# Performance work log

Hardware: AMD Instinct MI355X
Metric: run time of the kernel (lower is better)

Reference implementation:

```python
import jax, jax.numpy as jnp
import numpy as np

HEADS = 8
DIM_HEAD = 64
MAX_POS = 512


def setup_inputs() -> dict:
    key = jax.random.key(0)
    ks = jax.random.split(key, 10)
    b, n, dim, inner = 4, 1024, 512, HEADS * DIM_HEAD
    w = lambda k, shape: jax.random.normal(k, shape, jnp.float32) * 0.02
    return {
        "x": jax.random.normal(ks[0], (b, n, dim, 2), jnp.float32),
        "wq_r": w(ks[1], (dim, inner)),
        "wq_i": w(ks[2], (dim, inner)),
        "wkv_r": w(ks[3], (dim, 2 * inner)),
        "wkv_i": w(ks[4], (dim, 2 * inner)),
        "wo_r": w(ks[5], (inner, dim)),
        "wo_i": w(ks[6], (inner, dim)),
        "bo_r": w(ks[7], (dim,)),
        "bo_i": w(ks[8], (dim,)),
        "rel_emb": w(ks[9], (2 * MAX_POS + 1, DIM_HEAD)),
    }


def _clinear(t, Wr, Wi, br=None, bi=None):
    # complex linear: (a+ib)(Wr+iWi) = (aWr - bWi) + i(bWr + aWi)
    a, b = t[..., 0], t[..., 1]
    r = a @ Wr - b @ Wi
    i = b @ Wr + a @ Wi
    if br is not None:
        r = r + br
        i = i + bi
    return jnp.stack((r, i), axis=-1)


def _split_heads(t, h):
    # [b, n, h*d, 2] -> [b, h, n, d, 2]
    b, n, hd, c = t.shape
    return t.reshape(b, n, h, hd // h, c).transpose(0, 2, 1, 3, 4)


def reference(x, wq_r, wq_i, wkv_r, wkv_i, wo_r, wo_i, bo_r, bo_i, rel_emb):
    b, n = x.shape[0], x.shape[1]
    scale = DIM_HEAD ** (-0.5)

    q = _split_heads(_clinear(x, wq_r, wq_i), HEADS)          # [b,h,n,d,2]
    kv = _clinear(x, wkv_r, wkv_i)                            # [b,n,2*inner,2]
    k_, v_ = jnp.split(kv, 2, axis=-2)
    k = _split_heads(k_, HEADS)
    v = _split_heads(v_, HEADS)

    qr, qi = q[..., 0], q[..., 1]
    kr, ki = k[..., 0], k[..., 1]

    dots_r = (jnp.einsum('bhid,bhjd->bhij', qr, kr)
              - jnp.einsum('bhid,bhjd->bhij', qi, ki)) * scale
    dots_i = (jnp.einsum('bhid,bhjd->bhij', qr, ki)
              + jnp.einsum('bhid,bhjd->bhij', qi, kr)) * scale

    seq = jnp.arange(n)
    dist = jnp.clip(seq[:, None] - seq[None, :], -MAX_POS, MAX_POS) + MAX_POS  # [n,n]
    rel = rel_emb[dist]                                       # [n, n, d]
    dots_r = dots_r + jnp.einsum('bhnd,nrd->bhnr', qr, rel) * scale
    dots_i = dots_i + jnp.einsum('bhnd,nrd->bhnr', qi, rel) * scale

    # magnitude softmax over keys
    attn = jax.nn.softmax(jnp.sqrt(dots_r ** 2 + dots_i ** 2), axis=-1)  # [b,h,i,j]

    vr, vi = v[..., 0], v[..., 1]
    out_r = jnp.einsum('bhij,bhjd->bhid', attn, vr)
    out_i = jnp.einsum('bhij,bhjd->bhid', attn, vi)
    # [b,h,n,d] -> [b,n,h*d]
    out_r = out_r.transpose(0, 2, 1, 3).reshape(b, n, -1)
    out_i = out_i.transpose(0, 2, 1, 3).reshape(b, n, -1)
    out = jnp.stack((out_r, out_i), axis=-1)                  # [b,n,inner,2]

    # to_out (with bias); dropout prob 0 -> identity
    return _clinear(out, wo_r, wo_i, bo_r, bo_i)
```

## Files before the change

kernel.cpp:

```cpp
#include <hip/hip_runtime.h>
#include <hip/hip_bf16.h>


using bf16 = __bf16;
typedef __bf16 bf16x8 __attribute__((ext_vector_type(8)));
typedef float f32x4 __attribute__((ext_vector_type(4)));
typedef unsigned u32x4 __attribute__((ext_vector_type(4)));

#define MFMA16(a, b, c) __builtin_amdgcn_mfma_f32_16x16x32_bf16((a), (b), (c), 0, 0, 0)

__device__ __forceinline__ float ld_in(const void* p, long long i, int f32) {
  return f32 ? ((const float*)p)[i] : (float)((const bf16*)p)[i];
}

__device__ __forceinline__ void gl_lds16(const bf16* g, const bf16* l) {
  __builtin_amdgcn_global_load_lds(
      (const __attribute__((address_space(1))) void*)(unsigned long long)g,
      (__attribute__((address_space(3))) void*)(unsigned int)(unsigned long long)l,
      16, 0, 0);
}

template <int CTRL>
__device__ __forceinline__ float dpp_mv(float v) {
  int s = __builtin_bit_cast(int, v);
  return __builtin_bit_cast(float,
      __builtin_amdgcn_update_dpp(s, s, CTRL, 0xf, 0xf, false));
}
__device__ __forceinline__ float dpp_sum16(float v) {
  v += dpp_mv<0x121>(v);
  v += dpp_mv<0x122>(v);
  v += dpp_mv<0x124>(v);
  v += dpp_mv<0x128>(v);
  return v;
}

__device__ __forceinline__ unsigned pack_bf16(float lo, float hi) {
  unsigned a = (unsigned)__builtin_bit_cast(unsigned short, (bf16)lo);
  unsigned b = (unsigned)__builtin_bit_cast(unsigned short, (bf16)hi);
  return a | (b << 16);
}

__global__ __launch_bounds__(256) void k_diag(float* __restrict__ out, float v) {
  int idx = blockIdx.x * 256 + threadIdx.x;
  if (idx < 4194304) out[idx] = v;
}

__global__ void k_detect_all(
    const unsigned short* p0, const unsigned short* p1, const unsigned short* p2,
    const unsigned short* p3, const unsigned short* p4, const unsigned short* p5,
    const unsigned short* p6, const unsigned short* p7, const unsigned short* p8,
    const unsigned short* p9, int* __restrict__ flags) {
  static const int sizes[10] = {65536, 65536, 65536, 65536, 65536,
                                65536, 65536, 512, 512, 65536};
  const unsigned short* ptrs[10] = {p0, p1, p2, p3, p4, p5, p6, p7, p8, p9};
  __shared__ int cnt;
  if (threadIdx.x == 0) cnt = 0;
  __syncthreads();
  const int which = blockIdx.x;
  const unsigned short* p = ptrs[which];
  const int nhalf = sizes[which];
  const int ns = nhalf < 4096 ? nhalf : 4096;
  const int stp = nhalf / ns;
  int c = 0;
  for (int i = threadIdx.x; i < ns; i += 256) {
    const unsigned u = p[(size_t)i * stp];
    const unsigned e = (u >> 7) & 0xFF;
    if (e == 0xFF || (e < 64 && (u & 0x7FFF) != 0)) ++c;
  }
  atomicAdd(&cnt, c);
  __syncthreads();
  if (threadIdx.x == 0) flags[which] = (cnt > (ns >> 6)) ? 1 : 0;
}

__global__ __launch_bounds__(256) void k_build_all(
    const void* __restrict__ x,
    const void* __restrict__ wq_r, const void* __restrict__ wq_i,
    const void* __restrict__ wkv_r, const void* __restrict__ wkv_i,
    const void* __restrict__ wo_r, const void* __restrict__ wo_i,
    const void* __restrict__ rel,
    bf16* __restrict__ wct, bf16* __restrict__ wot,
    bf16* __restrict__ xd, bf16* __restrict__ rel_c,
    const int* __restrict__ flags) {
  __shared__ float tile[64][65];
  const int bid = blockIdx.x;
  const int t = threadIdx.x;
  if (bid < 1024) {
    const bool is_o = bid >= 768;
    const int lb = is_o ? bid - 768 : bid;
    const int k0 = (lb & 15) * 64;
    const int c0 = (lb >> 4) * 64;
    const int kk0 = k0 & 511;
    const bool hi = k0 >= 512;
    const void* src;
    int f, ld, scol;
    float sgn = 1.f;
    if (is_o) {
      ld = 512;
      if (c0 < 512) { scol = c0;       if (!hi) { src = wo_r; f = flags[5]; } else { src = wo_i; f = flags[6]; sgn = -1.f; } }
      else          { scol = c0 - 512; if (!hi) { src = wo_i; f = flags[6]; } else { src = wo_r; f = flags[5]; } }
    } else {
      ld = (c0 < 1024) ? 512 : 1024;
      if (c0 < 512)       { scol = c0;              if (!hi) { src = wq_r;  f = flags[1]; } else { src = wq_i;  f = flags[2]; sgn = -1.f; } }
      else if (c0 < 1024) { scol = c0 - 512;        if (!hi) { src = wq_i;  f = flags[2]; } else { src = wq_r;  f = flags[1]; } }
      else if (c0 < 1536) { scol = c0 - 1024;       if (!hi) { src = wkv_r; f = flags[3]; } else { src = wkv_i; f = flags[4]; sgn = -1.f; } }
      else if (c0 < 2048) { scol = c0 - 1536;       if (!hi) { src = wkv_i; f = flags[4]; } else { src = wkv_r; f = flags[3]; } }
      else if (c0 < 2560) { scol = c0 - 2048 + 512; if (!hi) { src = wkv_r; f = flags[3]; } else { src = wkv_i; f = flags[4]; sgn = -1.f; } }
      else                { scol = c0 - 2560 + 512; if (!hi) { src = wkv_i; f = flags[4]; } else { src = wkv_r; f = flags[3]; } }
    }
    const int cc = t & 63, rq = t >> 6;
#pragma unroll
    for (int rp = 0; rp < 16; ++rp) {
      const int rr = rp * 4 + rq;
      tile[rr][cc] = sgn * ld_in(src, (long long)(kk0 + rr) * ld + scol + cc, f);
    }
    __syncthreads();
    bf16* dst = is_o ? wot : wct;
    const int cr = t >> 3, kb = (t & 7) * 8;
#pragma unroll
    for (int p = 0; p < 2; ++p) {
      const int c = cr + p * 32;
      bf16x8 v;
#pragma unroll
      for (int e = 0; e < 8; ++e) v[e] = (bf16)tile[kb + e][c];
      *(bf16x8*)(dst + (size_t)(c0 + c) * 1024 + k0 + kb) = v;
    }
  } else if (bid < 9216) {
    const int f = flags[0];
    int idx = (bid - 1024) * 256 + t;
    int m = idx >> 9, j = idx & 511;
    long long base = (long long)m * 1024 + j * 2;
    xd[(size_t)m * 1024 + j] = (bf16)ld_in(x, base, f);
    xd[(size_t)m * 1024 + 512 + j] = (bf16)ld_in(x, base + 1, f);
  } else {
    const int f = flags[9];
    int idx = (bid - 9216) * 256 + t;
    if (idx < 65600) rel_c[idx] = (bf16)ld_in(rel, idx, f);
  }
}

template <int MODE, int BN>
__global__ __launch_bounds__(256) void k_gemm(
    const bf16* __restrict__ A, const bf16* __restrict__ Bt,
    bf16* __restrict__ C, float* __restrict__ Cf,
    bf16* __restrict__ Vtr, bf16* __restrict__ Vti,
    const int M, const int N, const int K,
    const void* __restrict__ bias_r, const void* __restrict__ bias_i,
    const int* __restrict__ flags) {
  constexpr int MT = (BN == 128) ? 4 : 2;
  __shared__ __align__(16) bf16 As[128 * 64];
  __shared__ __align__(16) bf16 Bs[BN * 64];
  const int tid = threadIdx.x;
  const int wave = tid >> 6, lane = tid & 63;
  const int lane15 = lane & 15, quad = lane >> 4;
  const int per = gridDim.x >> 3;
  const int s = (blockIdx.x & 7) * per + (blockIdx.x >> 3);
  const int nbx = N / BN;
  const int bm = (s / nbx) * 128, bn = (s % nbx) * BN;
  int wm, wn;
  if constexpr (BN == 128) { wm = (wave >> 1) * 64; wn = (wave & 1) * 64; }
  else                     { wm = wave * 32;        wn = 0; }
  const int sr = lane >> 3;
  const int scs = ((lane & 7) ^ sr) * 8;
  const int s7 = lane15 & 7;
  f32x4 acc[MT][4];
#pragma unroll
  for (int i = 0; i < MT; ++i)
#pragma unroll
    for (int j = 0; j < 4; ++j) acc[i][j] = (f32x4){0.f, 0.f, 0.f, 0.f};

  for (int k0 = 0; k0 < K; k0 += 64) {
#pragma unroll
    for (int p = 0; p < 4; ++p) {
      const int g = wave * 4 + p;
      gl_lds16(A + (size_t)(bm + g * 8 + sr) * K + k0 + scs, As + g * 512);
    }
    if constexpr (BN == 128) {
#pragma unroll
      for (int p = 0; p < 4; ++p) {
        const int g = wave * 4 + p;
        gl_lds16(Bt + (size_t)(bn + g * 8 + sr) * K + k0 + scs, Bs + g * 512);
      }
    } else {
#pragma unroll
      for (int p = 0; p < 2; ++p) {
        const int g = wave * 2 + p;
        gl_lds16(Bt + (size_t)(bn + g * 8 + sr) * K + k0 + scs, Bs + g * 512);
      }
    }
    __syncthreads();
#pragma unroll
    for (int kk = 0; kk < 2; ++kk) {
      const int go = ((kk * 4 + quad) ^ s7) * 8;
      bf16x8 af[MT], bfr[4];
#pragma unroll
      for (int mt = 0; mt < MT; ++mt)
        af[mt] = *(const bf16x8*)(As + (wm + mt * 16 + lane15) * 64 + go);
#pragma unroll
      for (int nt = 0; nt < 4; ++nt)
        bfr[nt] = *(const bf16x8*)(Bs + (wn + nt * 16 + lane15) * 64 + go);
#pragma unroll
      for (int mt = 0; mt < MT; ++mt)
#pragma unroll
        for (int nt = 0; nt < 4; ++nt) acc[mt][nt] = MFMA16(af[mt], bfr[nt], acc[mt][nt]);
    }
    __syncthreads();
  }

  if constexpr (MODE == 0) {
    if (bn < 2048) {
#pragma unroll
      for (int mt = 0; mt < MT; ++mt)
#pragma unroll
        for (int nt = 0; nt < 4; ++nt)
#pragma unroll
          for (int r = 0; r < 4; ++r) {
            const int m = bm + wm + mt * 16 + quad * 4 + r;
            const int n = bn + wn + nt * 16 + lane15;
            C[(size_t)m * 2048 + n] = (bf16)acc[mt][nt][r];
          }
    } else {
      const int hbase = bn - 2048 + wn;
      unsigned* vtp = (unsigned*)((hbase < 512) ? Vtr : Vti);
      const int dg0 = hbase & 511;
      const int bb = bm >> 10;
      const int jt = ((bm & 1023) >> 6) + (wm >> 6);
      const int bh = bb * 8 + (dg0 >> 6);
      unsigned* slab = vtp + (((size_t)(bh * 16 + jt)) << 11) + (quad * 16 + lane15) * 4;
#pragma unroll
      for (int nt = 0; nt < 4; ++nt)
#pragma unroll
        for (int hp = 0; hp < 2; ++hp) {
          u32x4 w;
#pragma unroll
          for (int r = 0; r < 4; ++r)
            w[r] = pack_bf16(acc[2 * hp][nt][r], acc[2 * hp + 1][nt][r]);
          *(u32x4*)(slab + nt * 512 + hp * 256) = w;
        }
    }
  } else {
    const int fbr = flags[7], fbi = flags[8];
#pragma unroll
    for (int mt = 0; mt < MT; ++mt)
#pragma unroll
      for (int nt = 0; nt < 4; ++nt)
#pragma unroll
        for (int r = 0; r < 4; ++r) {
          const int m = bm + wm + mt * 16 + quad * 4 + r;
          const int n = bn + wn + nt * 16 + lane15;
          float v = acc[mt][nt][r];
          const int c = (n < 512) ? n : n - 512;
          v += ld_in((n < 512) ? bias_r : bias_i, c, (n < 512) ? fbr : fbi);
          Cf[(size_t)m * 1024 + c * 2 + ((n < 512) ? 0 : 1)] = v;
        }
  }
}

__device__ __forceinline__ bf16x8 lds_frag72(const bf16* base, int row, int kofs) {
  return *(const bf16x8*)(base + row * 72 + kofs);
}

__global__ __launch_bounds__(256, 2) void k_attn(
    const bf16* __restrict__ C1, const bf16* __restrict__ vt_r, const bf16* __restrict__ vt_i,
    const bf16* __restrict__ rel, bf16* __restrict__ Oc) {
  __shared__ __align__(16) bf16 kr_s[64 * 72];
  __shared__ __align__(16) bf16 ki_s[64 * 72];
  __shared__ unsigned Gt32[4][1360];

  const int tid = threadIdx.x;
  const int wave = tid >> 6, lane = tid & 63;
  const int lane15 = lane & 15, quad = lane >> 4;
  const int qk0 = quad * 8;
  const int bid0 = blockIdx.x;
  const int bid = (bid0 & 7) * 64 + (bid0 >> 3);
  const int bh = bid >> 4, it = bid & 15;
  const int b = bh >> 3, h = bh & 7;
  const int i0 = it * 64;
  const int tq = tid >> 3;
  const int tc = (tid & 7) * 8;

  unsigned* const Gw = &Gt32[wave][0];

  const size_t qbase = (size_t)(b * 1024 + i0 + wave * 16 + lane15) * 2048 + h * 64;
  bf16x8 aqr[2], aqi[2], aqin[2];
  aqr[0] = *(const bf16x8*)(C1 + qbase + qk0);
  aqr[1] = *(const bf16x8*)(C1 + qbase + 32 + qk0);
  aqi[0] = *(const bf16x8*)(C1 + qbase + 512 + qk0);
  aqi[1] = *(const bf16x8*)(C1 + qbase + 512 + 32 + qk0);
#pragma unroll
  for (int c = 0; c < 2; ++c)
#pragma unroll
    for (int e = 0; e < 8; ++e) aqin[c][e] = (bf16)(-(float)aqi[c][e]);

  f32x4 o_r[4], o_i[4];
#pragma unroll
  for (int dt = 0; dt < 4; ++dt) { o_r[dt] = (f32x4){0.f,0.f,0.f,0.f}; o_i[dt] = (f32x4){0.f,0.f,0.f,0.f}; }
  f32x4 l_st = (f32x4){0.f, 0.f, 0.f, 0.f};

  bf16x8 pKr[2], pKi[2];
  auto issueK = [&](int jtn) {
    const int j0 = jtn * 64;
#pragma unroll
    for (int p = 0; p < 2; ++p) {
      const int row = p * 32 + tq;
      const size_t gbase = (size_t)(b * 1024 + j0 + row) * 2048 + h * 64 + tc;
      pKr[p] = *(const bf16x8*)(C1 + gbase + 1024);
      pKi[p] = *(const bf16x8*)(C1 + gbase + 1536);
    }
  };

  bf16x8 rb0[5], rb1[5];
  auto loadR = [&](int jtn) {
    const int t0w = 449 + i0 - jtn * 64 + wave * 16;
#pragma unroll
    for (int g = 0; g < 5; ++g) {
      int trw = t0w + g * 16 + lane15;
      trw = trw < 0 ? 0 : (trw > 1024 ? 1024 : trw);
      const bf16* rp = rel + (size_t)trw * 64;
      rb0[g] = *(const bf16x8*)(rp + qk0);
      rb1[g] = *(const bf16x8*)(rp + 32 + qk0);
    }
  };

  issueK(0);
  loadR(0);
  for (int jt = 0; jt < 16; ++jt) {
#pragma unroll
    for (int p = 0; p < 2; ++p) {
      const int row = p * 32 + tq;
      *(bf16x8*)(kr_s + row * 72 + tc) = pKr[p];
      *(bf16x8*)(ki_s + row * 72 + tc) = pKi[p];
    }
    __syncthreads();
    if (jt < 15) issueK(jt + 1);

#pragma unroll
    for (int g = 0; g < 5; ++g) {
      f32x4 gr = (f32x4){0.f,0.f,0.f,0.f}, gi = (f32x4){0.f,0.f,0.f,0.f};
      gr = MFMA16(aqr[0], rb0[g], gr);
      gr = MFMA16(aqr[1], rb1[g], gr);
      gi = MFMA16(aqi[0], rb0[g], gi);
      gi = MFMA16(aqi[1], rb1[g], gi);
      const int trow = (g * 16 + lane15) * 17;
#pragma unroll
      for (int r = 0; r < 4; ++r)
        Gw[trow + quad * 4 + r] = pack_bf16(gr[r], gi[r]);
    }

    if (jt < 15) loadR(jt + 1);

    f32x4 s_r[4], s_i[4];
#pragma unroll
    for (int ct = 0; ct < 4; ++ct) { s_r[ct] = (f32x4){0.f,0.f,0.f,0.f}; s_i[ct] = (f32x4){0.f,0.f,0.f,0.f}; }
    __builtin_amdgcn_s_setprio(1);
#pragma unroll
    for (int ct = 0; ct < 4; ++ct) {
      const int krow = ct * 16 + lane15;
      bf16x8 bkr0 = lds_frag72(kr_s, krow, qk0), bkr1 = lds_frag72(kr_s, krow, 32 + qk0);
      bf16x8 bki0 = lds_frag72(ki_s, krow, qk0), bki1 = lds_frag72(ki_s, krow, 32 + qk0);
      s_r[ct] = MFMA16(aqr[0], bkr0, s_r[ct]);
      s_r[ct] = MFMA16(aqr[1], bkr1, s_r[ct]);
      s_r[ct] = MFMA16(aqin[0], bki0, s_r[ct]);
      s_r[ct] = MFMA16(aqin[1], bki1, s_r[ct]);
      s_i[ct] = MFMA16(aqr[0], bki0, s_i[ct]);
      s_i[ct] = MFMA16(aqr[1], bki1, s_i[ct]);
      s_i[ct] = MFMA16(aqi[0], bkr0, s_i[ct]);
      s_i[ct] = MFMA16(aqi[1], bkr1, s_i[ct]);
    }
    __builtin_amdgcn_s_setprio(0);
    __syncthreads();

    const unsigned* vbr = (const unsigned*)vt_r + (((size_t)(bh * 16 + jt)) << 11) + lane * 4;
    const unsigned* vbi = (const unsigned*)vt_i + (((size_t)(bh * 16 + jt)) << 11) + lane * 4;
    bf16x8 vr0[4], vr1[4];
#pragma unroll
    for (int dt = 0; dt < 4; ++dt) {
      vr0[dt] = *(const bf16x8*)(vbr + dt * 512);
      vr1[dt] = *(const bf16x8*)(vbr + dt * 512 + 256);
    }

    float mag[4][4];
#pragma unroll
    for (int ct = 0; ct < 4; ++ct) {
      const int jj = ct * 16 + lane15;
#pragma unroll
      for (int r = 0; r < 4; ++r) {
        const int ii = quad * 4 + r;
        const unsigned gv = Gw[(ii - jj + 63) * 17 + ii];
        const float gr = __builtin_bit_cast(float, gv << 16);
        const float gi = __builtin_bit_cast(float, gv & 0xffff0000u);
        const float dr = s_r[ct][r] + gr;
        const float di = s_i[ct][r] + gi;
        mag[ct][r] = fminf(0.125f * sqrtf(dr * dr + di * di), 80.f);
      }
    }
#pragma unroll
    for (int r = 0; r < 4; ++r) {
      const int ii = quad * 4 + r;
      float pv[4];
#pragma unroll
      for (int ct = 0; ct < 4; ++ct) pv[ct] = __expf(mag[ct][r]);
      l_st[r] += (pv[0] + pv[1]) + (pv[2] + pv[3]);
      Gw[ii * 36 + lane15]      = pack_bf16(pv[0], pv[1]);
      Gw[ii * 36 + 16 + lane15] = pack_bf16(pv[2], pv[3]);
    }

    bf16x8 vi0[4], vi1[4];
#pragma unroll
    for (int dt = 0; dt < 4; ++dt) {
      vi0[dt] = *(const bf16x8*)(vbi + dt * 512);
      vi1[dt] = *(const bf16x8*)(vbi + dt * 512 + 256);
    }

    bf16x8 ap0 = *(const bf16x8*)((const bf16*)Gw + lane15 * 72 + quad * 8);
    bf16x8 ap1 = *(const bf16x8*)((const bf16*)Gw + lane15 * 72 + 32 + quad * 8);
    __builtin_amdgcn_s_setprio(1);
#pragma unroll
    for (int dt = 0; dt < 4; ++dt) {
      o_r[dt] = MFMA16(ap0, vr0[dt], o_r[dt]);
      o_r[dt] = MFMA16(ap1, vr1[dt], o_r[dt]);
    }
#pragma unroll
    for (int dt = 0; dt < 4; ++dt) {
      o_i[dt] = MFMA16(ap0, vi0[dt], o_i[dt]);
      o_i[dt] = MFMA16(ap1, vi1[dt], o_i[dt]);
    }
    __builtin_amdgcn_s_setprio(0);
  }

  const size_t obase = (size_t)(b * 1024 + i0 + wave * 16) * 1024 + h * 64;
#pragma unroll
  for (int r = 0; r < 4; ++r) {
    const float inv = 1.0f / dpp_sum16(l_st[r]);
    const int ii = quad * 4 + r;
#pragma unroll
    for (int dt = 0; dt < 4; ++dt) {
      Oc[obase + (size_t)ii * 1024 + dt * 16 + lane15] = (bf16)(o_r[dt][r] * inv);
      Oc[obase + (size_t)ii * 1024 + 512 + dt * 16 + lane15] = (bf16)(o_i[dt][r] * inv);
    }
  }
}

extern "C" void kernel_launch(void* const* d_in, const int* in_sizes, int n_in,
                              void* d_out, int out_size, void* d_ws, size_t ws_size,
                              hipStream_t stream) {
  float* out = (float*)d_out;

  if (n_in != 10) { k_diag<<<16384, 256, 0, stream>>>(out, 300000.f); return; }
  if (out_size != 4194304) { k_diag<<<16384, 256, 0, stream>>>(out, 400000.f); return; }
  static const int dict_sizes[10] = {4194304, 262144, 262144, 524288, 524288,
                                     262144, 262144, 512, 512, 65600};
  for (int i = 0; i < 10; ++i) {
    if (in_sizes[i] != dict_sizes[i]) { k_diag<<<16384, 256, 0, stream>>>(out, 200000.f); return; }
  }
  const size_t NEED = 50462888;
  if (ws_size < NEED) { k_diag<<<16384, 256, 0, stream>>>(out, 100000.f); return; }

  const void* x     = d_in[0];
  const void* wq_r  = d_in[1];
  const void* wq_i  = d_in[2];
  const void* wkv_r = d_in[3];
  const void* wkv_i = d_in[4];
  const void* wo_r  = d_in[5];
  const void* wo_i  = d_in[6];
  const void* bo_r  = d_in[7];
  const void* bo_i  = d_in[8];
  const void* rel   = d_in[9];

  char* ws = (char*)d_ws;
  bf16* C1   = (bf16*)(ws);
  bf16* Vtr  = (bf16*)(ws + 16777216);
  bf16* Vti  = (bf16*)(ws + 20971520);
  bf16* Xd   = (bf16*)(ws + 25165824);
  bf16* Oc   = (bf16*)(ws + 33554432);
  bf16* WcT  = (bf16*)(ws + 41943040);
  bf16* WoT  = (bf16*)(ws + 48234496);
  bf16* relc = (bf16*)(ws + 50331648);
  int*  flags= (int*)(ws + 50462848);

  k_detect_all<<<10, 256, 0, stream>>>(
      (const unsigned short*)x, (const unsigned short*)wq_r, (const unsigned short*)wq_i,
      (const unsigned short*)wkv_r, (const unsigned short*)wkv_i, (const unsigned short*)wo_r,
      (const unsigned short*)wo_i, (const unsigned short*)bo_r, (const unsigned short*)bo_i,
      (const unsigned short*)rel, flags);

  k_build_all<<<9473, 256, 0, stream>>>(x, wq_r, wq_i, wkv_r, wkv_i, wo_r, wo_i, rel,
                                        WcT, WoT, Xd, relc, flags);

  k_gemm<0, 128><<<768, 256, 0, stream>>>(Xd, WcT, C1, nullptr, Vtr, Vti,
                                          4096, 3072, 1024, nullptr, nullptr, flags);
  k_attn<<<512, 256, 0, stream>>>(C1, Vtr, Vti, relc, Oc);
  k_gemm<1, 64><<<512, 256, 0, stream>>>(Oc, WoT, nullptr, out, nullptr, nullptr,
                                         4096, 1024, 1024, bo_r, bo_i, flags);
}
```

Baseline: 223.4 us.

## Shrink output GEMM tiles, simplify softmax exponent, reduce dtype-probe sampling

New measurement: 221.7 us. No clear change (-0.8%).

```diff
diff --git a/kernel.cpp b/kernel.cpp
--- a/kernel.cpp
+++ b/kernel.cpp
@@ -59,7 +59,7 @@
   const int which = blockIdx.x;
   const unsigned short* p = ptrs[which];
   const int nhalf = sizes[which];
-  const int ns = nhalf < 4096 ? nhalf : 4096;
+  const int ns = nhalf < 1024 ? nhalf : 1024;
   const int stp = nhalf / ns;
   int c = 0;
   for (int i = threadIdx.x; i < ns; i += 256) {
@@ -138,7 +138,7 @@
   }
 }
 
-template <int MODE, int BN>
+template <int MODE, int BM, int BN>
 __global__ __launch_bounds__(256) void k_gemm(
     const bf16* __restrict__ A, const bf16* __restrict__ Bt,
     bf16* __restrict__ C, float* __restrict__ Cf,
@@ -146,8 +146,10 @@
     const int M, const int N, const int K,
     const void* __restrict__ bias_r, const void* __restrict__ bias_i,
     const int* __restrict__ flags) {
-  constexpr int MT = (BN == 128) ? 4 : 2;
-  __shared__ __align__(16) bf16 As[128 * 64];
+  constexpr int MT = (BM == 128 && BN == 128) ? 4 : (BM == 128 ? 2 : 1);
+  constexpr int APW = (BM / 8) / 4;
+  constexpr int BPW = (BN / 8) / 4;
+  __shared__ __align__(16) bf16 As[BM * 64];
   __shared__ __align__(16) bf16 Bs[BN * 64];
   const int tid = threadIdx.x;
   const int wave = tid >> 6, lane = tid & 63;
@@ -155,10 +157,11 @@
   const int per = gridDim.x >> 3;
   const int s = (blockIdx.x & 7) * per + (blockIdx.x >> 3);
   const int nbx = N / BN;
-  const int bm = (s / nbx) * 128, bn = (s % nbx) * BN;
+  const int bm = (s / nbx) * BM, bn = (s % nbx) * BN;
   int wm, wn;
-  if constexpr (BN == 128) { wm = (wave >> 1) * 64; wn = (wave & 1) * 64; }
-  else                     { wm = wave * 32;        wn = 0; }
+  if constexpr (BM == 128 && BN == 128) { wm = (wave >> 1) * 64; wn = (wave & 1) * 64; }
+  else if constexpr (BM == 128)         { wm = wave * 32;        wn = 0; }
+  else                                  { wm = wave * 16;        wn = 0; }
   const int sr = lane >> 3;
   const int scs = ((lane & 7) ^ sr) * 8;
   const int s7 = lane15 & 7;
@@ -170,22 +173,14 @@
 
   for (int k0 = 0; k0 < K; k0 += 64) {
 #pragma unroll
-    for (int p = 0; p < 4; ++p) {
-      const int g = wave * 4 + p;
+    for (int p = 0; p < APW; ++p) {
+      const int g = wave * APW + p;
       gl_lds16(A + (size_t)(bm + g * 8 + sr) * K + k0 + scs, As + g * 512);
     }
-    if constexpr (BN == 128) {
-#pragma unroll
-      for (int p = 0; p < 4; ++p) {
-        const int g = wave * 4 + p;
-        gl_lds16(Bt + (size_t)(bn + g * 8 + sr) * K + k0 + scs, Bs + g * 512);
-      }
-    } else {
-#pragma unroll
-      for (int p = 0; p < 2; ++p) {
-        const int g = wave * 2 + p;
-        gl_lds16(Bt + (size_t)(bn + g * 8 + sr) * K + k0 + scs, Bs + g * 512);
-      }
+#pragma unroll
+    for (int p = 0; p < BPW; ++p) {
+      const int g = wave * BPW + p;
+      gl_lds16(Bt + (size_t)(bn + g * 8 + sr) * K + k0 + scs, Bs + g * 512);
     }
     __syncthreads();
 #pragma unroll
@@ -390,7 +385,7 @@
         const float gi = __builtin_bit_cast(float, gv & 0xffff0000u);
         const float dr = s_r[ct][r] + gr;
         const float di = s_i[ct][r] + gi;
-        mag[ct][r] = fminf(0.125f * sqrtf(dr * dr + di * di), 80.f);
+        mag[ct][r] = sqrtf(dr * dr + di * di);
       }
     }
 #pragma unroll
@@ -398,7 +393,7 @@
       const int ii = quad * 4 + r;
       float pv[4];
 #pragma unroll
-      for (int ct = 0; ct < 4; ++ct) pv[ct] = __expf(mag[ct][r]);
+      for (int ct = 0; ct < 4; ++ct) pv[ct] = exp2f(0.18033688f * mag[ct][r]);
       l_st[r] += (pv[0] + pv[1]) + (pv[2] + pv[3]);
       Gw[ii * 36 + lane15]      = pack_bf16(pv[0], pv[1]);
       Gw[ii * 36 + 16 + lane15] = pack_bf16(pv[2], pv[3]);
@@ -486,9 +481,9 @@
   k_build_all<<<9473, 256, 0, stream>>>(x, wq_r, wq_i, wkv_r, wkv_i, wo_r, wo_i, rel,
                                         WcT, WoT, Xd, relc, flags);
 
-  k_gemm<0, 128><<<768, 256, 0, stream>>>(Xd, WcT, C1, nullptr, Vtr, Vti,
-                                          4096, 3072, 1024, nullptr, nullptr, flags);
+  k_gemm<0, 128, 128><<<768, 256, 0, stream>>>(Xd, WcT, C1, nullptr, Vtr, Vti,
+                                               4096, 3072, 1024, nullptr, nullptr, flags);
   k_attn<<<512, 256, 0, stream>>>(C1, Vtr, Vti, relc, Oc);
-  k_gemm<1, 64><<<512, 256, 0, stream>>>(Oc, WoT, nullptr, out, nullptr, nullptr,
-                                         4096, 1024, 1024, bo_r, bo_i, flags);
-}
+  k_gemm<1, 64, 64><<<1024, 256, 0, stream>>>(Oc, WoT, nullptr, out, nullptr, nullptr,
+                                              4096, 1024, 1024, bo_r, bo_i, flags);
+}
```
